# Performance work log

Measured on AMD Instinct MI355X. Metric: run time of the kernel, lower is better.

Reference implementation:

```python
import jax, jax.numpy as jnp
import numpy as np

B, S, D, H, TB = 8, 512, 512, 8, 64
DK = D // H
SCALE = DK ** -0.5


def setup_inputs() -> dict:
    key = jax.random.key(0)
    ks = jax.random.split(key, 9)
    return {
        "query_input": jax.random.normal(ks[0], (B, S, D), jnp.float32),
        "key_input": jax.random.normal(ks[1], (B, S, D), jnp.float32),
        "batch_temporal_mat": jax.random.uniform(ks[2], (B, S, S), jnp.float32) * 100.0,
        "Wq": jax.random.normal(ks[3], (D, D), jnp.float32) * (D ** -0.5),
        "Wk": jax.random.normal(ks[4], (D, D), jnp.float32) * (D ** -0.5),
        "Wv": jax.random.normal(ks[5], (D, D), jnp.float32) * (D ** -0.5),
        "Wp": jax.random.normal(ks[6], (D, D), jnp.float32) * (D ** -0.5),
        "Wt1": jax.random.normal(ks[7], (1, TB), jnp.float32),
        "Wt2": jax.random.normal(ks[8], (TB, 1), jnp.float32) * (TB ** -0.5),
    }


def _split_heads(x):
    # [B,S,D] -> [B,H,S,DK]
    b, s, _ = x.shape
    return x.reshape(b, s, H, DK).transpose(0, 2, 1, 3)


def reference(query_input, key_input, batch_temporal_mat, Wq, Wk, Wv, Wp, Wt1, Wt2):
    q = _split_heads(query_input @ Wq)   # [B,H,S,DK]
    k = _split_heads(key_input @ Wk)
    v = _split_heads(key_input @ Wv)

    scores = jnp.einsum("bhqd,bhkd->bhqk", q, k) * SCALE  # [B,H,S,S]

    # temporal bias: 1/log(e + t) -> Dense(TB) -> leaky_relu(0.2) -> Dense(1)
    t = 1.0 / jnp.log(jnp.e + batch_temporal_mat)          # [B,S,S]
    h = t[..., None] * Wt1[0]                              # [B,S,S,TB] (Dense from 1 dim)
    h = jnp.where(h >= 0, h, 0.2 * h)                      # leaky_relu alpha=0.2
    bias = (h @ Wt2)[..., 0]                               # [B,S,S]
    scores = scores + bias[:, None]                        # broadcast over heads

    attn = jax.nn.softmax(scores, axis=-1)
    out = jnp.einsum("bhqk,bhkd->bhqd", attn, v)           # [B,H,S,DK]
    out = out.transpose(0, 2, 1, 3).reshape(query_input.shape[0], -1, D)
    return out @ Wp
```

## Files before the change

### kernel.cpp

```cpp
#include <hip/hip_runtime.h>

#define NB 8
#define NS 512
#define ND 512
#define NH 8
#define NDK 64
#define NTB 64
#define SCALE_F 0.125f

typedef short s16x8 __attribute__((ext_vector_type(8)));
typedef float floatx4 __attribute__((ext_vector_type(4)));

__device__ __forceinline__ unsigned short bf16rn(float x) {
  unsigned u = __builtin_bit_cast(unsigned, x);
  u += 0x7FFFu + ((u >> 16) & 1u);
  return (unsigned short)(u >> 16);
}
__device__ __forceinline__ s16x8 ld8(const unsigned short* p) {
  return *reinterpret_cast<const s16x8*>(p);
}
__device__ __forceinline__ floatx4 mfma16(s16x8 a, s16x8 b, floatx4 c) {
  return __builtin_amdgcn_mfma_f32_16x16x32_bf16(a, b, c, 0, 0, 0);
}

#define GLOAD16(g, l)                                                          \
  __builtin_amdgcn_global_load_lds(                                            \
      (const __attribute__((address_space(1))) unsigned int*)(g),              \
      (__attribute__((address_space(3))) unsigned int*)(l), 16, 0, 0)

__device__ __forceinline__ s16x8 frag(const unsigned short* plane, int row, int chunk) {
  return *reinterpret_cast<const s16x8*>(plane + row * 64 + ((chunk ^ (row & 7)) * 8));
}



__global__ __launch_bounds__(256) void prep_kernel(
    const float* __restrict__ xq, const float* __restrict__ xk,
    const float* __restrict__ tmat, const float* __restrict__ Wq,
    const float* __restrict__ Wk, const float* __restrict__ Wv,
    const float* __restrict__ Wp, const float* __restrict__ wt1,
    const float* __restrict__ wt2, unsigned short* __restrict__ xq_bf,
    unsigned short* __restrict__ xk_bf, unsigned short* __restrict__ wT,
    unsigned short* __restrict__ biasf) {
  __shared__ float tile[64][65];
  __shared__ float w1[NTB], w2[NTB];
  const int bid = blockIdx.x;

  if (bid < 256) {
    int wi = bid >> 6;
    int t = bid & 63;
    int n0 = (t >> 3) * 64, k0 = (t & 7) * 64;
    const float* Wsrc = (wi == 0) ? Wq : (wi == 1) ? Wk : (wi == 2) ? Wv : Wp;
    unsigned short* dst = wT + (size_t)wi * ND * ND;
    int tx = threadIdx.x & 63, ty = threadIdx.x >> 6;
#pragma unroll
    for (int rr = 0; rr < 16; rr++) {
      int k = rr * 4 + ty;
      tile[k][tx] = Wsrc[(size_t)(k0 + k) * ND + n0 + tx];
    }
    __syncthreads();
#pragma unroll
    for (int rr = 0; rr < 16; rr++) {
      int n = rr * 4 + ty;
      dst[(size_t)(n0 + n) * ND + k0 + tx] = bf16rn(tile[tx][n]);
    }
  } else if (bid < 768) {
    const int per = NB * NS * ND / 4;
    for (int t = (bid - 256) * 256 + (int)threadIdx.x; t < 2 * per; t += 512 * 256) {
      const float4* src;
      unsigned short* dst;
      int i;
      if (t < per) { src = (const float4*)xq; dst = xq_bf; i = t; }
      else         { src = (const float4*)xk; dst = xk_bf; i = t - per; }
      float4 v = src[i];
      ushort4 o;
      o.x = bf16rn(v.x); o.y = bf16rn(v.y);
      o.z = bf16rn(v.z); o.w = bf16rn(v.w);
      ((ushort4*)dst)[i] = o;
    }
  } else {
    if (threadIdx.x < NTB) {
      w1[threadIdx.x] = wt1[threadIdx.x];
      w2[threadIdx.x] = wt2[threadIdx.x];
    }
    __syncthreads();
    float C = 0.f;
#pragma unroll 16
    for (int j = 0; j < NTB; j++) {
      float a = w1[j];
      C += (a >= 0.f ? a : 0.2f * a) * w2[j];
    }
    const int total = NB * NS * NS / 4;
    const float E = 2.718281828459045f;
    for (int t = (bid - 768) * 256 + (int)threadIdx.x; t < total; t += 512 * 256) {
      float4 T = ((const float4*)tmat)[t];
      ushort4 o;
      o.x = __builtin_bit_cast(unsigned short, (_Float16)(C / logf(E + T.x)));
      o.y = __builtin_bit_cast(unsigned short, (_Float16)(C / logf(E + T.y)));
      o.z = __builtin_bit_cast(unsigned short, (_Float16)(C / logf(E + T.z)));
      o.w = __builtin_bit_cast(unsigned short, (_Float16)(C / logf(E + T.w)));
      ((ushort4*)biasf)[t] = o;
    }
  }
}


__global__ __launch_bounds__(256) void gemm_qkv_kernel(
    const unsigned short* __restrict__ xq_bf, const unsigned short* __restrict__ xk_bf,
    const unsigned short* __restrict__ wT, unsigned short* __restrict__ Qd,
    unsigned short* __restrict__ Kd, unsigned short* __restrict__ Vt) {
  const int z = blockIdx.z;
  const unsigned short* Ag = (z == 0) ? xq_bf : xk_bf;
  const unsigned short* Bg = wT + (size_t)z * ND * ND;
  const int m0 = blockIdx.y * 128, n0 = blockIdx.x * 128;
  const int lane = threadIdx.x & 63, w = threadIdx.x >> 6;
  const int c = lane & 15, g = lane >> 4;
  const int wm = (w >> 1) * 64, wn = (w & 1) * 64;
  const int r8 = lane >> 3, ck = lane & 7;

  __shared__ __align__(16) unsigned short Ah[128 * 64];
  __shared__ __align__(16) unsigned short Bh[128 * 64];

  floatx4 acc[4][4];
#pragma unroll
  for (int i = 0; i < 4; i++)
#pragma unroll
    for (int j = 0; j < 4; j++) acc[i][j] = (floatx4){0.f, 0.f, 0.f, 0.f};

  for (int ks = 0; ks < ND; ks += 64) {
    __syncthreads();
#pragma unroll
    for (int t = 0; t < 4; t++) {
      int row = w * 32 + t * 8 + r8;
      int sw = (ck ^ (row & 7)) * 8;
      GLOAD16(Ag + (size_t)(m0 + row) * ND + ks + sw, Ah + (w * 32 + t * 8) * 64);
      GLOAD16(Bg + (size_t)(n0 + row) * ND + ks + sw, Bh + (w * 32 + t * 8) * 64);
    }
    __syncthreads();
#pragma unroll
    for (int hf = 0; hf < 2; hf++) {
      s16x8 af[4], bf[4];
#pragma unroll
      for (int i = 0; i < 4; i++) af[i] = frag(Ah, wm + i * 16 + c, hf * 4 + g);
#pragma unroll
      for (int j = 0; j < 4; j++) bf[j] = frag(Bh, wn + j * 16 + c, hf * 4 + g);
      if (z != 2) {
#pragma unroll
        for (int i = 0; i < 4; i++)
#pragma unroll
          for (int j = 0; j < 4; j++) acc[i][j] = mfma16(af[i], bf[j], acc[i][j]);
      } else {
#pragma unroll
        for (int i = 0; i < 4; i++)
#pragma unroll
          for (int j = 0; j < 4; j++) acc[i][j] = mfma16(bf[j], af[i], acc[i][j]);
      }
    }
  }

  if (z != 2) {
    const float sc = (z == 0) ? SCALE_F : 1.0f;
    unsigned short* D = (z == 0) ? Qd : Kd;
#pragma unroll
    for (int i = 0; i < 4; i++)
#pragma unroll
      for (int j = 0; j < 4; j++) {
        int row0 = m0 + wm + i * 16 + g * 4;
        int col = n0 + wn + j * 16 + c;
        int h2 = col >> 6, dk = col & 63;
#pragma unroll
        for (int r = 0; r < 4; r++) {
          int rr = row0 + r;
          int bb = rr >> 9, s = rr & 511;
          D[(((size_t)bb * NH + h2) * NS + s) * NDK + dk] = bf16rn(acc[i][j][r] * sc);
        }
      }
  } else {
#pragma unroll
    for (int i = 0; i < 4; i++)
#pragma unroll
      for (int j = 0; j < 4; j++) {
        int n_base = n0 + wn + j * 16 + g * 4;
        int m = m0 + wm + i * 16 + c;
        int bb = m >> 9, s = m & 511;
#pragma unroll
        for (int r = 0; r < 4; r++) {
          int n = n_base + r;
          int h2 = n >> 6, dk = n & 63;
          Vt[(((size_t)bb * NH + h2) * NDK + dk) * NS + s] = bf16rn(acc[i][j][r]);
        }
      }
  }
}

__global__ __launch_bounds__(256) void gemm_out_kernel(
    const unsigned short* __restrict__ AO, const unsigned short* __restrict__ wT,
    float* __restrict__ out) {
  const unsigned short* Bg = wT + (size_t)3 * ND * ND;
  const int m0 = blockIdx.y * 128, n0 = blockIdx.x * 128;
  const int lane = threadIdx.x & 63, w = threadIdx.x >> 6;
  const int c = lane & 15, g = lane >> 4;
  const int wm = (w >> 1) * 64, wn = (w & 1) * 64;
  const int r8 = lane >> 3, ck = lane & 7;

  __shared__ __align__(16) unsigned short Ah[128 * 64];
  __shared__ __align__(16) unsigned short Bh[128 * 64];

  floatx4 acc[4][4];
#pragma unroll
  for (int i = 0; i < 4; i++)
#pragma unroll
    for (int j = 0; j < 4; j++) acc[i][j] = (floatx4){0.f, 0.f, 0.f, 0.f};

  for (int ks = 0; ks < ND; ks += 64) {
    __syncthreads();
#pragma unroll
    for (int t = 0; t < 4; t++) {
      int row = w * 32 + t * 8 + r8;
      int sw = (ck ^ (row & 7)) * 8;
      GLOAD16(AO + (size_t)(m0 + row) * ND + ks + sw, Ah + (w * 32 + t * 8) * 64);
      GLOAD16(Bg + (size_t)(n0 + row) * ND + ks + sw, Bh + (w * 32 + t * 8) * 64);
    }
    __syncthreads();
#pragma unroll
    for (int hf = 0; hf < 2; hf++) {
      s16x8 af[4], bf[4];
#pragma unroll
      for (int i = 0; i < 4; i++) af[i] = frag(Ah, wm + i * 16 + c, hf * 4 + g);
#pragma unroll
      for (int j = 0; j < 4; j++) bf[j] = frag(Bh, wn + j * 16 + c, hf * 4 + g);
#pragma unroll
      for (int i = 0; i < 4; i++)
#pragma unroll
        for (int j = 0; j < 4; j++) acc[i][j] = mfma16(af[i], bf[j], acc[i][j]);
    }
  }

#pragma unroll
  for (int i = 0; i < 4; i++)
#pragma unroll
    for (int j = 0; j < 4; j++) {
      int row0 = m0 + wm + i * 16 + g * 4;
      int col = n0 + wn + j * 16 + c;
#pragma unroll
      for (int r = 0; r < 4; r++)
        out[(size_t)(row0 + r) * ND + col] = acc[i][j][r];
    }
}


__global__ __launch_bounds__(256) void attn_kernel(
    const unsigned short* __restrict__ Qd, const unsigned short* __restrict__ Kd,
    const unsigned short* __restrict__ Vt, const unsigned short* __restrict__ biasf,
    unsigned short* __restrict__ AO) {
  const int id = blockIdx.x;
  const int hh = id & 7, b = (id >> 3) & 7, qt = id >> 6;
  const int lane = threadIdx.x & 63, w = threadIdx.x >> 6;
  const int c = lane & 15, g = lane >> 4;
  const size_t hoff = ((size_t)b * NH + hh) * NS * NDK;
  const unsigned short* Kb = Kd + hoff;
  const unsigned short* Vb = Vt + hoff;
  const int qbase = qt * 16;
  const _Float16* bp = (const _Float16*)biasf;

  __shared__ __align__(16) char shmem[15360];
  unsigned short* Pw = (unsigned short*)shmem + w * (16 * 72);
  float* scratch = (float*)shmem;

  s16x8 qf[2];
  {
    const unsigned short* Qb = Qd + hoff;
    size_t off = (size_t)(qbase + c) * NDK + g * 8;
    qf[0] = ld8(Qb + off);
    qf[1] = ld8(Qb + off + 32);
  }

  floatx4 acc_o[4];
#pragma unroll
  for (int d = 0; d < 4; d++) acc_o[d] = (floatx4){0.f, 0.f, 0.f, 0.f};
  float ps[4] = {0.f, 0.f, 0.f, 0.f};

#pragma unroll
  for (int kt = 0; kt < 2; kt++) {
    const int key0 = w * 128 + kt * 64;
    float bb[4][4];
#pragma unroll
    for (int f = 0; f < 4; f++)
#pragma unroll
      for (int r = 0; r < 4; r++)
        bb[f][r] = (float)bp[((size_t)b * NS + qbase + g * 4 + r) * NS + key0 + f * 16 + c];

    floatx4 sc[4];
#pragma unroll
    for (int f = 0; f < 4; f++) {
      const unsigned short* kp = Kb + (size_t)(key0 + f * 16 + c) * NDK + g * 8;
      s16x8 k0 = ld8(kp);
      s16x8 k1 = ld8(kp + 32);
      floatx4 zz = (floatx4){0.f, 0.f, 0.f, 0.f};
      zz = mfma16(qf[0], k0, zz);
      sc[f] = mfma16(qf[1], k1, zz);
    }

#pragma unroll
    for (int f = 0; f < 4; f++)
#pragma unroll
      for (int r = 0; r < 4; r++) {
        float p = __expf(sc[f][r] + bb[f][r]);
        ps[r] += p;
        Pw[(g * 4 + r) * 72 + f * 16 + c] = bf16rn(p);
      }

#pragma unroll
    for (int kf = 0; kf < 2; kf++) {
      s16x8 pf = *reinterpret_cast<const s16x8*>(&Pw[c * 72 + kf * 32 + g * 8]);
#pragma unroll
      for (int d = 0; d < 4; d++) {
        s16x8 vf = ld8(Vb + (size_t)(d * 16 + c) * NS + key0 + kf * 32 + g * 8);
        acc_o[d] = mfma16(pf, vf, acc_o[d]);
      }
    }
  }

  __syncthreads();
  if (w > 0) {
    float* s = scratch + (size_t)(w - 1) * 20 * 64;
#pragma unroll
    for (int d = 0; d < 4; d++)
#pragma unroll
      for (int r = 0; r < 4; r++) s[(d * 4 + r) * 64 + lane] = acc_o[d][r];
#pragma unroll
    for (int r = 0; r < 4; r++) s[(16 + r) * 64 + lane] = ps[r];
  }
  __syncthreads();
  if (w == 0) {
#pragma unroll
    for (int ww = 0; ww < 3; ww++) {
      const float* s = scratch + (size_t)ww * 20 * 64;
#pragma unroll
      for (int d = 0; d < 4; d++)
#pragma unroll
        for (int r = 0; r < 4; r++) acc_o[d][r] += s[(d * 4 + r) * 64 + lane];
#pragma unroll
      for (int r = 0; r < 4; r++) ps[r] += s[(16 + r) * 64 + lane];
    }
#pragma unroll
    for (int r = 0; r < 4; r++) {
#pragma unroll
      for (int mask = 1; mask < 16; mask <<= 1)
        ps[r] += __shfl_xor(ps[r], mask, 64);
    }
#pragma unroll
    for (int r = 0; r < 4; r++) {
      float inv = 1.0f / ps[r];
      int qrow = qbase + g * 4 + r;
#pragma unroll
      for (int d = 0; d < 4; d++)
        AO[((size_t)b * NS + qrow) * ND + hh * NDK + d * 16 + c] =
            bf16rn(acc_o[d][r] * inv);
    }
  }
}


extern "C" void kernel_launch(void* const* d_in, const int* in_sizes, int n_in,
                              void* d_out, int out_size, void* d_ws, size_t ws_size,
                              hipStream_t stream) {
  const float* xq = (const float*)d_in[0];
  const float* xk = (const float*)d_in[1];
  const float* tmat = (const float*)d_in[2];
  const float* Wq = (const float*)d_in[3];
  const float* Wk = (const float*)d_in[4];
  const float* Wv = (const float*)d_in[5];
  const float* Wp = (const float*)d_in[6];
  const float* Wt1 = (const float*)d_in[7];
  const float* Wt2 = (const float*)d_in[8];
  float* out = (float*)d_out;

  char* ws = (char*)d_ws;
  const size_t MB = 1u << 20;
  unsigned short* xq_bf = (unsigned short*)(ws + 0 * MB);
  unsigned short* xk_bf = (unsigned short*)(ws + 4 * MB);
  unsigned short* wT = (unsigned short*)(ws + 8 * MB);
  unsigned short* biasf = (unsigned short*)(ws + 10 * MB);
  unsigned short* Qd = (unsigned short*)(ws + 14 * MB);
  unsigned short* Kd = (unsigned short*)(ws + 18 * MB);
  unsigned short* Vt = (unsigned short*)(ws + 22 * MB);
  unsigned short* AO = (unsigned short*)(ws + 26 * MB);

  prep_kernel<<<1280, 256, 0, stream>>>(xq, xk, tmat, Wq, Wk, Wv, Wp, Wt1, Wt2,
                                        xq_bf, xk_bf, wT, biasf);
  gemm_qkv_kernel<<<dim3(4, 32, 3), 256, 0, stream>>>(xq_bf, xk_bf, wT, Qd, Kd, Vt);
  attn_kernel<<<2048, 256, 0, stream>>>(Qd, Kd, Vt, biasf, AO);
  gemm_out_kernel<<<dim3(4, 32), 256, 0, stream>>>(AO, wT, out);
}
```

Baseline: 147.8 us.

## Transpose bias layout and process 32 query rows per attention block

```diff
diff --git a/kernel.cpp b/kernel.cpp
--- a/kernel.cpp
+++ b/kernel.cpp
@@ -10,6 +10,7 @@
 
 typedef short s16x8 __attribute__((ext_vector_type(8)));
 typedef float floatx4 __attribute__((ext_vector_type(4)));
+typedef _Float16 f16x4 __attribute__((ext_vector_type(4)));
 
 __device__ __forceinline__ unsigned short bf16rn(float x) {
   unsigned u = __builtin_bit_cast(unsigned, x);
@@ -31,7 +32,6 @@
 __device__ __forceinline__ s16x8 frag(const unsigned short* plane, int row, int chunk) {
   return *reinterpret_cast<const s16x8*>(plane + row * 64 + ((chunk ^ (row & 7)) * 8));
 }
-
 
 
 __global__ __launch_bounds__(256) void prep_kernel(
@@ -41,7 +41,7 @@
     const float* __restrict__ Wp, const float* __restrict__ wt1,
     const float* __restrict__ wt2, unsigned short* __restrict__ xq_bf,
     unsigned short* __restrict__ xk_bf, unsigned short* __restrict__ wT,
-    unsigned short* __restrict__ biasf) {
+    unsigned short* __restrict__ biasT) {
   __shared__ float tile[64][65];
   __shared__ float w1[NTB], w2[NTB];
   const int bid = blockIdx.x;
@@ -90,16 +90,22 @@
       float a = w1[j];
       C += (a >= 0.f ? a : 0.2f * a) * w2[j];
     }
-    const int total = NB * NS * NS / 4;
     const float E = 2.718281828459045f;
-    for (int t = (bid - 768) * 256 + (int)threadIdx.x; t < total; t += 512 * 256) {
-      float4 T = ((const float4*)tmat)[t];
-      ushort4 o;
-      o.x = __builtin_bit_cast(unsigned short, (_Float16)(C / logf(E + T.x)));
-      o.y = __builtin_bit_cast(unsigned short, (_Float16)(C / logf(E + T.y)));
-      o.z = __builtin_bit_cast(unsigned short, (_Float16)(C / logf(E + T.z)));
-      o.w = __builtin_bit_cast(unsigned short, (_Float16)(C / logf(E + T.w)));
-      ((ushort4*)biasf)[t] = o;
+    int t = bid - 768;
+    int b = t >> 6;
+    int q0 = ((t >> 3) & 7) * 64, k0 = (t & 7) * 64;
+    int tx = threadIdx.x & 63, ty = threadIdx.x >> 6;
+#pragma unroll
+    for (int rr = 0; rr < 16; rr++) {
+      int q = rr * 4 + ty;
+      tile[q][tx] = C / logf(E + tmat[((size_t)b * NS + q0 + q) * NS + k0 + tx]);
+    }
+    __syncthreads();
+#pragma unroll
+    for (int rr = 0; rr < 16; rr++) {
+      int k = rr * 4 + ty;
+      biasT[((size_t)b * NS + k0 + k) * NS + q0 + tx] =
+          __builtin_bit_cast(unsigned short, (_Float16)tile[tx][k]);
     }
   }
 }
@@ -251,7 +257,7 @@
 
 __global__ __launch_bounds__(256) void attn_kernel(
     const unsigned short* __restrict__ Qd, const unsigned short* __restrict__ Kd,
-    const unsigned short* __restrict__ Vt, const unsigned short* __restrict__ biasf,
+    const unsigned short* __restrict__ Vt, const unsigned short* __restrict__ biasT,
     unsigned short* __restrict__ AO) {
   const int id = blockIdx.x;
   const int hh = id & 7, b = (id >> 3) & 7, qt = id >> 6;
@@ -260,104 +266,128 @@
   const size_t hoff = ((size_t)b * NH + hh) * NS * NDK;
   const unsigned short* Kb = Kd + hoff;
   const unsigned short* Vb = Vt + hoff;
-  const int qbase = qt * 16;
-  const _Float16* bp = (const _Float16*)biasf;
-
-  __shared__ __align__(16) char shmem[15360];
-  unsigned short* Pw = (unsigned short*)shmem + w * (16 * 72);
+  const int qbase = qt * 32;
+
+  __shared__ __align__(16) char shmem[30720];
+  unsigned short* Pw = (unsigned short*)shmem + w * (32 * 72);
   float* scratch = (float*)shmem;
 
-  s16x8 qf[2];
-  {
-    const unsigned short* Qb = Qd + hoff;
-    size_t off = (size_t)(qbase + c) * NDK + g * 8;
-    qf[0] = ld8(Qb + off);
-    qf[1] = ld8(Qb + off + 32);
-  }
-
-  floatx4 acc_o[4];
-#pragma unroll
-  for (int d = 0; d < 4; d++) acc_o[d] = (floatx4){0.f, 0.f, 0.f, 0.f};
-  float ps[4] = {0.f, 0.f, 0.f, 0.f};
+  s16x8 qf[2][2];
+#pragma unroll
+  for (int rg = 0; rg < 2; rg++) {
+    size_t off = (size_t)(qbase + rg * 16 + c) * NDK + g * 8;
+    qf[rg][0] = ld8(Qd + hoff + off);
+    qf[rg][1] = ld8(Qd + hoff + off + 32);
+  }
+
+  floatx4 acc_o[2][4];
+#pragma unroll
+  for (int rg = 0; rg < 2; rg++)
+#pragma unroll
+    for (int d = 0; d < 4; d++) acc_o[rg][d] = (floatx4){0.f, 0.f, 0.f, 0.f};
+  float ps[2][4] = {{0.f, 0.f, 0.f, 0.f}, {0.f, 0.f, 0.f, 0.f}};
 
 #pragma unroll
   for (int kt = 0; kt < 2; kt++) {
     const int key0 = w * 128 + kt * 64;
-    float bb[4][4];
+
+    f16x4 bb[2][4];
 #pragma unroll
     for (int f = 0; f < 4; f++)
 #pragma unroll
-      for (int r = 0; r < 4; r++)
-        bb[f][r] = (float)bp[((size_t)b * NS + qbase + g * 4 + r) * NS + key0 + f * 16 + c];
-
-    floatx4 sc[4];
+      for (int rg = 0; rg < 2; rg++)
+        bb[rg][f] = *reinterpret_cast<const f16x4*>(
+            biasT + ((size_t)b * NS + key0 + f * 16 + c) * NS + qbase + rg * 16 + g * 4);
+
+    floatx4 sc[2][4];
 #pragma unroll
     for (int f = 0; f < 4; f++) {
       const unsigned short* kp = Kb + (size_t)(key0 + f * 16 + c) * NDK + g * 8;
       s16x8 k0 = ld8(kp);
       s16x8 k1 = ld8(kp + 32);
-      floatx4 zz = (floatx4){0.f, 0.f, 0.f, 0.f};
-      zz = mfma16(qf[0], k0, zz);
-      sc[f] = mfma16(qf[1], k1, zz);
-    }
-
-#pragma unroll
-    for (int f = 0; f < 4; f++)
-#pragma unroll
-      for (int r = 0; r < 4; r++) {
-        float p = __expf(sc[f][r] + bb[f][r]);
-        ps[r] += p;
-        Pw[(g * 4 + r) * 72 + f * 16 + c] = bf16rn(p);
-      }
+#pragma unroll
+      for (int rg = 0; rg < 2; rg++) {
+        floatx4 zz = (floatx4){0.f, 0.f, 0.f, 0.f};
+        zz = mfma16(qf[rg][0], k0, zz);
+        sc[rg][f] = mfma16(qf[rg][1], k1, zz);
+      }
+    }
+
+#pragma unroll
+    for (int rg = 0; rg < 2; rg++)
+#pragma unroll
+      for (int f = 0; f < 4; f++)
+#pragma unroll
+        for (int r = 0; r < 4; r++) {
+          float p = __expf(sc[rg][f][r] + (float)bb[rg][f][r]);
+          ps[rg][r] += p;
+          Pw[(rg * 16 + g * 4 + r) * 72 + f * 16 + c] = bf16rn(p);
+        }
 
 #pragma unroll
     for (int kf = 0; kf < 2; kf++) {
-      s16x8 pf = *reinterpret_cast<const s16x8*>(&Pw[c * 72 + kf * 32 + g * 8]);
-#pragma unroll
-      for (int d = 0; d < 4; d++) {
-        s16x8 vf = ld8(Vb + (size_t)(d * 16 + c) * NS + key0 + kf * 32 + g * 8);
-        acc_o[d] = mfma16(pf, vf, acc_o[d]);
+      s16x8 vf[4];
+#pragma unroll
+      for (int d = 0; d < 4; d++)
+        vf[d] = ld8(Vb + (size_t)(d * 16 + c) * NS + key0 + kf * 32 + g * 8);
+#pragma unroll
+      for (int rg = 0; rg < 2; rg++) {
+        s16x8 pf = *reinterpret_cast<const s16x8*>(&Pw[(rg * 16 + c) * 72 + kf * 32 + g * 8]);
+#pragma unroll
+        for (int d = 0; d < 4; d++) acc_o[rg][d] = mfma16(pf, vf[d], acc_o[rg][d]);
       }
     }
   }
 
   __syncthreads();
   if (w > 0) {
-    float* s = scratch + (size_t)(w - 1) * 20 * 64;
-#pragma unroll
-    for (int d = 0; d < 4; d++)
-#pragma unroll
-      for (int r = 0; r < 4; r++) s[(d * 4 + r) * 64 + lane] = acc_o[d][r];
-#pragma unroll
-    for (int r = 0; r < 4; r++) s[(16 + r) * 64 + lane] = ps[r];
+    float* s = scratch + (size_t)(w - 1) * 40 * 64;
+#pragma unroll
+    for (int rg = 0; rg < 2; rg++) {
+#pragma unroll
+      for (int d = 0; d < 4; d++)
+#pragma unroll
+        for (int r = 0; r < 4; r++)
+          s[(rg * 20 + d * 4 + r) * 64 + lane] = acc_o[rg][d][r];
+#pragma unroll
+      for (int r = 0; r < 4; r++) s[(rg * 20 + 16 + r) * 64 + lane] = ps[rg][r];
+    }
   }
   __syncthreads();
   if (w == 0) {
 #pragma unroll
     for (int ww = 0; ww < 3; ww++) {
-      const float* s = scratch + (size_t)ww * 20 * 64;
-#pragma unroll
-      for (int d = 0; d < 4; d++)
-#pragma unroll
-        for (int r = 0; r < 4; r++) acc_o[d][r] += s[(d * 4 + r) * 64 + lane];
-#pragma unroll
-      for (int r = 0; r < 4; r++) ps[r] += s[(16 + r) * 64 + lane];
-    }
-#pragma unroll
-    for (int r = 0; r < 4; r++) {
-#pragma unroll
-      for (int mask = 1; mask < 16; mask <<= 1)
-        ps[r] += __shfl_xor(ps[r], mask, 64);
-    }
-#pragma unroll
-    for (int r = 0; r < 4; r++) {
-      float inv = 1.0f / ps[r];
-      int qrow = qbase + g * 4 + r;
-#pragma unroll
-      for (int d = 0; d < 4; d++)
-        AO[((size_t)b * NS + qrow) * ND + hh * NDK + d * 16 + c] =
-            bf16rn(acc_o[d][r] * inv);
-    }
+      const float* s = scratch + (size_t)ww * 40 * 64;
+#pragma unroll
+      for (int rg = 0; rg < 2; rg++) {
+#pragma unroll
+        for (int d = 0; d < 4; d++)
+#pragma unroll
+          for (int r = 0; r < 4; r++)
+            acc_o[rg][d][r] += s[(rg * 20 + d * 4 + r) * 64 + lane];
+#pragma unroll
+        for (int r = 0; r < 4; r++) ps[rg][r] += s[(rg * 20 + 16 + r) * 64 + lane];
+      }
+    }
+#pragma unroll
+    for (int rg = 0; rg < 2; rg++)
+#pragma unroll
+      for (int r = 0; r < 4; r++) {
+#pragma unroll
+        for (int mask = 1; mask < 16; mask <<= 1)
+          ps[rg][r] += __shfl_xor(ps[rg][r], mask, 64);
+      }
+#pragma unroll
+    for (int rg = 0; rg < 2; rg++)
+#pragma unroll
+      for (int r = 0; r < 4; r++) {
+        float inv = 1.0f / ps[rg][r];
+        int qrow = qbase + rg * 16 + g * 4 + r;
+#pragma unroll
+        for (int d = 0; d < 4; d++)
+          AO[((size_t)b * NS + qrow) * ND + hh * NDK + d * 16 + c] =
+              bf16rn(acc_o[rg][d][r] * inv);
+      }
   }
 }
 
@@ -381,15 +411,15 @@
   unsigned short* xq_bf = (unsigned short*)(ws + 0 * MB);
   unsigned short* xk_bf = (unsigned short*)(ws + 4 * MB);
   unsigned short* wT = (unsigned short*)(ws + 8 * MB);
-  unsigned short* biasf = (unsigned short*)(ws + 10 * MB);
+  unsigned short* biasT = (unsigned short*)(ws + 10 * MB);
   unsigned short* Qd = (unsigned short*)(ws + 14 * MB);
   unsigned short* Kd = (unsigned short*)(ws + 18 * MB);
   unsigned short* Vt = (unsigned short*)(ws + 22 * MB);
   unsigned short* AO = (unsigned short*)(ws + 26 * MB);
 
   prep_kernel<<<1280, 256, 0, stream>>>(xq, xk, tmat, Wq, Wk, Wv, Wp, Wt1, Wt2,
-                                        xq_bf, xk_bf, wT, biasf);
+                                        xq_bf, xk_bf, wT, biasT);
   gemm_qkv_kernel<<<dim3(4, 32, 3), 256, 0, stream>>>(xq_bf, xk_bf, wT, Qd, Kd, Vt);
-  attn_kernel<<<2048, 256, 0, stream>>>(Qd, Kd, Vt, biasf, AO);
+  attn_kernel<<<1024, 256, 0, stream>>>(Qd, Kd, Vt, biasT, AO);
   gemm_out_kernel<<<dim3(4, 32), 256, 0, stream>>>(AO, wT, out);
 }
```

After: 141.3 us. -4.4%, faster.
